# Optimization experiments

Measured on AMD Instinct MI355X. Metric: run time of the kernel, lower is better.

Reference implementation:

```python
import jax, jax.numpy as jnp
import numpy as np

PASS = 8        # pass_through_size
FLOW = 16       # flow_size
TRANS = FLOW - PASS  # transform_size = 8
NBINS = 64
HID = 1024


def _conditioner(yA, w1, b1, w2, b2, w3, b3):
    # MLP producing unnormalized positive bin widths Q: [B, TRANS, NBINS]
    h = jax.nn.relu(yA @ w1 + b1)
    h = jax.nn.relu(h @ w2 + b2)
    q = jax.nn.softplus(h @ w3 + b3) + 1e-6  # positivity for slopes
    return q.reshape(-1, TRANS, NBINS)


def setup_inputs() -> dict:
    key = jax.random.key(0)
    ks = jax.random.split(key, 4)
    B = 65536
    y = jax.random.uniform(ks[0], (B, FLOW + 1), dtype=jnp.float32)
    w1 = jax.random.normal(ks[1], (PASS, HID), dtype=jnp.float32) / np.sqrt(PASS)
    w2 = jax.random.normal(ks[2], (HID, HID), dtype=jnp.float32) / np.sqrt(HID)
    w3 = jax.random.normal(ks[3], (HID, TRANS * NBINS), dtype=jnp.float32) / np.sqrt(HID)
    return {
        "y": y,
        "w1": w1, "b1": jnp.zeros((HID,), jnp.float32),
        "w2": w2, "b2": jnp.zeros((HID,), jnp.float32),
        "w3": w3, "b3": jnp.zeros((TRANS * NBINS,), jnp.float32),
    }


def reference(y, w1, b1, w2, b2, w3, b3):
    yA = y[:, :PASS]                      # [B, PASS]
    yB = y[:, PASS:FLOW]                  # [B, TRANS]
    jac = y[:, FLOW:FLOW + 1]             # [B, 1]

    Q = _conditioner(yA, w1, b1, w2, b2, w3, b3)  # [B, TRANS, NBINS]
    Qsum = jnp.cumsum(Q, axis=-1)
    Qnorms = Qsum[:, :, -1:]
    Q = Q / (Qnorms / NBINS)              # slopes per bin
    Qsum = Qsum / Qnorms                  # normalized CDF knots (last == 1)

    # searchsorted(side='left') per row: count of knots strictly below value
    ybins = jnp.sum(Qsum < yB[..., None], axis=-1)          # [B, TRANS] int32
    ybins = jnp.clip(ybins, 0, NBINS - 1)                   # guard fp edge case

    paddedQsum = jnp.pad(Qsum, ((0, 0), (0, 0), (1, 0)))    # prepend 0 knot
    offsets = jnp.take_along_axis(paddedQsum, ybins[..., None], axis=-1)[..., 0]
    slopes = jnp.take_along_axis(Q, ybins[..., None], axis=-1)[..., 0]

    xB = (yB - offsets) / slopes + ybins.astype(jnp.float32) / NBINS
    jac = jac * jnp.prod(1.0 / slopes, axis=-1, keepdims=True)
    return jnp.concatenate((yA, xB, jac), axis=-1)          # [B, FLOW+1]
```

## Files before the change

kernel.cpp:

```cpp
#include <hip/hip_runtime.h>
#include <hip/hip_bf16.h>
#include <hip/hip_fp16.h>

#define HID 1024
#define QCOLS 512

typedef _Float16 f16x8 __attribute__((ext_vector_type(8)));
typedef float f32x4 __attribute__((ext_vector_type(4)));

__global__ void tconv_split(const float* __restrict__ src, __half* __restrict__ hi,
                            __half* __restrict__ lo, int K, int N, float scale) {
  __shared__ float tile[32][33];
  int n0 = blockIdx.x * 32, k0 = blockIdx.y * 32;
  int tx = threadIdx.x, ty = threadIdx.y;
  for (int i = ty; i < 32; i += 8)
    tile[i][tx] = src[(size_t)(k0 + i) * N + n0 + tx];
  __syncthreads();
  for (int i = ty; i < 32; i += 8) {
    float v = tile[tx][i] * scale;
    __half h = __float2half(v);
    size_t o = (size_t)(n0 + i) * K + k0 + tx;
    hi[o] = h;
    lo[o] = __float2half(v - __half2float(h));
  }
}

__global__ __launch_bounds__(256)
void h1_split(const float* __restrict__ y, const float* __restrict__ w1,
              const float* __restrict__ b1, __half* __restrict__ hi,
              __half* __restrict__ lo, int row0, int nrows) {
  int idx = blockIdx.x * 256 + threadIdx.x;
  if (idx >= nrows * HID) return;
  int r = idx >> 10, c = idx & (HID - 1);
  const float* yr = y + (size_t)(row0 + r) * 17;
  float acc = b1[c];
#pragma unroll
  for (int k = 0; k < 8; ++k) acc = fmaf(yr[k], w1[k * HID + c], acc);
  float v = fmaxf(acc, 0.f) * 64.f;
  __half h = __float2half(v);
  size_t o = (size_t)r * HID + c;
  hi[o] = h;
  lo[o] = __float2half(v - __half2float(h));
}

template <int ACT>
__global__ __launch_bounds__(256)
void gemm_split(const __half* __restrict__ Ahi, const __half* __restrict__ Alo,
                const __half* __restrict__ Bhi, const __half* __restrict__ Blo,
                const float* __restrict__ bias, __half* __restrict__ Chi,
                __half* __restrict__ Clo, float* __restrict__ Cf,
                int M, int N, int K) {
  __shared__ __half lds[4][128 * 32];
  const int tid = threadIdx.x;
  const int wave = tid >> 6, lane = tid & 63;
  const int wr = (wave >> 1) * 64, wc = (wave & 1) * 64;
  const size_t row_blk = (size_t)blockIdx.y * 128;
  const size_t col_blk = (size_t)blockIdx.x * 128;

  f32x4 acc[4][4] = {};

  const int rr_l = lane >> 2;
  const int kk_l = (lane & 3) * 8;

  for (int kt = 0; kt < K; kt += 32) {
    __syncthreads();
#pragma unroll
    for (int j = 0; j < 2; ++j) {
      const int c = wave * 2 + j;
      const int rr = c * 16 + rr_l;
      const size_t ga = (row_blk + rr) * (size_t)K + kt + kk_l;
      const size_t gb = (col_blk + rr) * (size_t)K + kt + kk_l;
      const int lo_off = c * 1024 + lane * 16;
      __builtin_amdgcn_global_load_lds((__attribute__((address_space(1))) void*)(Ahi + ga),
                                       (__attribute__((address_space(3))) void*)((char*)&lds[0][0] + lo_off), 16, 0, 0);
      __builtin_amdgcn_global_load_lds((__attribute__((address_space(1))) void*)(Alo + ga),
                                       (__attribute__((address_space(3))) void*)((char*)&lds[1][0] + lo_off), 16, 0, 0);
      __builtin_amdgcn_global_load_lds((__attribute__((address_space(1))) void*)(Bhi + gb),
                                       (__attribute__((address_space(3))) void*)((char*)&lds[2][0] + lo_off), 16, 0, 0);
      __builtin_amdgcn_global_load_lds((__attribute__((address_space(1))) void*)(Blo + gb),
                                       (__attribute__((address_space(3))) void*)((char*)&lds[3][0] + lo_off), 16, 0, 0);
    }
    __syncthreads();

    const int kb = (lane >> 4) * 16;
    f16x8 ah[4], al[4], bh[4], bl[4];
#pragma unroll
    for (int m = 0; m < 4; ++m) {
      const int rb = (wr + m * 16 + (lane & 15)) * 64 + kb;
      ah[m] = *(const f16x8*)((const char*)&lds[0][0] + rb);
      al[m] = *(const f16x8*)((const char*)&lds[1][0] + rb);
    }
#pragma unroll
    for (int n = 0; n < 4; ++n) {
      const int rb = (wc + n * 16 + (lane & 15)) * 64 + kb;
      bh[n] = *(const f16x8*)((const char*)&lds[2][0] + rb);
      bl[n] = *(const f16x8*)((const char*)&lds[3][0] + rb);
    }
#pragma unroll
    for (int m = 0; m < 4; ++m)
#pragma unroll
      for (int n = 0; n < 4; ++n) {
        acc[m][n] = __builtin_amdgcn_mfma_f32_16x16x32_f16(ah[m], bh[n], acc[m][n], 0, 0, 0);
        acc[m][n] = __builtin_amdgcn_mfma_f32_16x16x32_f16(ah[m], bl[n], acc[m][n], 0, 0, 0);
        acc[m][n] = __builtin_amdgcn_mfma_f32_16x16x32_f16(al[m], bh[n], acc[m][n], 0, 0, 0);
      }
  }

  const float unscale = 1.f / 16384.f;
#pragma unroll
  for (int m = 0; m < 4; ++m) {
    const size_t row_b = row_blk + wr + m * 16 + (lane >> 4) * 4;
#pragma unroll
    for (int n = 0; n < 4; ++n) {
      const size_t col = col_blk + wc + n * 16 + (lane & 15);
      const float bv = bias[col];
#pragma unroll
      for (int j = 0; j < 4; ++j) {
        float v = acc[m][n][j] * unscale + bv;
        const size_t o = (row_b + j) * (size_t)N + col;
        if constexpr (ACT == 0) {
          float r = fmaxf(v, 0.f) * 64.f;
          __half h = __float2half(r);
          Chi[o] = h;
          Clo[o] = __float2half(r - __half2float(h));
        } else {
          float sp = fmaxf(v, 0.f) + log1pf(expf(-fabsf(v)));
          Cf[o] = sp + 1e-6f;
        }
      }
    }
  }
}

__global__ __launch_bounds__(256)
void epilogue_kernel(const float* __restrict__ y, const float* __restrict__ q,
                     float* __restrict__ out, int row0, int nrows) {
  const int wave = threadIdx.x >> 6, lane = threadIdx.x & 63;
  const int r = blockIdx.x * 4 + wave;
  if (r >= nrows) return;
  const float* yr = y + (size_t)(row0 + r) * 17;
  float* orow = out + (size_t)(row0 + r) * 17;
  const float* qr = q + (size_t)r * QCOLS;
  float prod_inv = 1.f;
#pragma unroll
  for (int t = 0; t < 8; ++t) {
    const float qv = qr[t * 64 + lane];
    float s = qv;
#pragma unroll
    for (int d = 1; d < 64; d <<= 1) {
      float u = __shfl_up(s, d);
      if (lane >= d) s += u;
    }
    const float total = __shfl(s, 63);
    const float sn = s / total;
    const float dnorm = total * 0.015625f;
    const float slope_l = qv / dnorm;
    const float yb = yr[8 + t];
    const unsigned long long m = __ballot(sn < yb);
    int bin = (int)__popcll(m);
    bin = bin > 63 ? 63 : bin;
    const float off_g = __shfl(sn, bin > 0 ? bin - 1 : 0);
    const float off = (bin == 0) ? 0.f : off_g;
    const float sl = __shfl(slope_l, bin);
    const float xB = (yb - off) / sl + (float)bin * 0.015625f;
    if (lane == t) orow[8 + t] = xB;
    prod_inv *= (1.f / sl);
  }
  if (lane < 8) orow[lane] = yr[lane];
  if (lane == 8) orow[16] = yr[16] * prod_inv;
}

extern "C" void kernel_launch(void* const* d_in, const int* in_sizes, int n_in,
                              void* d_out, int out_size, void* d_ws, size_t ws_size,
                              hipStream_t stream) {
  const float* y  = (const float*)d_in[0];
  const float* w1 = (const float*)d_in[1];
  const float* b1 = (const float*)d_in[2];
  const float* w2 = (const float*)d_in[3];
  const float* b2 = (const float*)d_in[4];
  const float* w3 = (const float*)d_in[5];
  const float* b3 = (const float*)d_in[6];
  float* out = (float*)d_out;
  const long Btot = in_sizes[0] / 17;

  char* ws = (char*)d_ws;
  __half* w2thi = (__half*)ws;
  __half* w2tlo = (__half*)(ws + (2u << 20));
  __half* w3thi = (__half*)(ws + (4u << 20));
  __half* w3tlo = (__half*)(ws + (5u << 20));
  const size_t fixed = (size_t)6 << 20;

  size_t avail = ws_size > fixed ? ws_size - fixed : 0;
  long maxrows = (long)(avail / 8192);
  long chunk = Btot < maxrows ? Btot : maxrows;
  chunk &= ~127L;
  if (chunk < 128) chunk = 128;

  __half* h1hi = (__half*)(ws + fixed);
  __half* h1lo = (__half*)(ws + fixed + (size_t)chunk * 2048);
  __half* h2hi = (__half*)(ws + fixed + (size_t)chunk * 4096);
  __half* h2lo = (__half*)(ws + fixed + (size_t)chunk * 6144);
  float* qbuf = (float*)h1hi;

  dim3 tb(32, 8);
  tconv_split<<<dim3(HID / 32, HID / 32), tb, 0, stream>>>(w2, w2thi, w2tlo, HID, HID, 256.f);
  tconv_split<<<dim3(QCOLS / 32, HID / 32), tb, 0, stream>>>(w3, w3thi, w3tlo, HID, QCOLS, 256.f);

  for (long row0 = 0; row0 < Btot; row0 += chunk) {
    const int nr = (int)((Btot - row0 < chunk) ? (Btot - row0) : chunk);
    h1_split<<<nr * (HID / 256), 256, 0, stream>>>(y, w1, b1, h1hi, h1lo, (int)row0, nr);
    gemm_split<0><<<dim3(HID / 128, nr / 128), 256, 0, stream>>>(
        h1hi, h1lo, w2thi, w2tlo, b2, h2hi, h2lo, nullptr, nr, HID, HID);
    gemm_split<1><<<dim3(QCOLS / 128, nr / 128), 256, 0, stream>>>(
        h2hi, h2lo, w3thi, w3tlo, b3, nullptr, nullptr, qbuf, nr, QCOLS, HID);
    epilogue_kernel<<<(nr + 3) / 4, 256, 0, stream>>>(y, qbuf, out, (int)row0, nr);
  }
}
```

Baseline: 1.061 ms.

## Rewrite split-fp16 GEMMs as 256x256 double-buffered kernel with interleaved hi/lo layout

Stores the hi and lo fp16 halves of activations and weights interleaved along K (row stride 2048), so the three-product split GEMM becomes a single K=3072 loop over concatenated segments (hi*hi, hi*lo, lo*hi). The new kernel uses 256x256 tiles with 512 threads, double-buffered LDS with XOR swizzling, async global-to-LDS loads overlapped with MFMA, s_setprio, and XCD-aware block remapping. The goal is more data reuse per tile, hiding load latency and avoiding LDS bank conflicts. In exchange it needs 128KB of LDS and heavy register use, and chunks must be multiples of 256 rows.

```diff
diff --git a/kernel.cpp b/kernel.cpp
--- a/kernel.cpp
+++ b/kernel.cpp
@@ -1,15 +1,16 @@
 #include <hip/hip_runtime.h>
-#include <hip/hip_bf16.h>
 #include <hip/hip_fp16.h>
 
 #define HID 1024
 #define QCOLS 512
+#define KP 2048
+#define NT 48
 
 typedef _Float16 f16x8 __attribute__((ext_vector_type(8)));
 typedef float f32x4 __attribute__((ext_vector_type(4)));
 
-__global__ void tconv_split(const float* __restrict__ src, __half* __restrict__ hi,
-                            __half* __restrict__ lo, int K, int N, float scale) {
+__global__ void tconv_split(const float* __restrict__ src, __half* __restrict__ dst,
+                            int K, int N, float scale) {
   __shared__ float tile[32][33];
   int n0 = blockIdx.x * 32, k0 = blockIdx.y * 32;
   int tx = threadIdx.x, ty = threadIdx.y;
@@ -19,16 +20,16 @@
   for (int i = ty; i < 32; i += 8) {
     float v = tile[tx][i] * scale;
     __half h = __float2half(v);
-    size_t o = (size_t)(n0 + i) * K + k0 + tx;
-    hi[o] = h;
-    lo[o] = __float2half(v - __half2float(h));
+    size_t o = (size_t)(n0 + i) * (2 * K) + k0 + tx;
+    dst[o] = h;
+    dst[o + K] = __float2half(v - __half2float(h));
   }
 }
 
 __global__ __launch_bounds__(256)
 void h1_split(const float* __restrict__ y, const float* __restrict__ w1,
-              const float* __restrict__ b1, __half* __restrict__ hi,
-              __half* __restrict__ lo, int row0, int nrows) {
+              const float* __restrict__ b1, __half* __restrict__ h1,
+              int row0, int nrows) {
   int idx = blockIdx.x * 256 + threadIdx.x;
   if (idx >= nrows * HID) return;
   int r = idx >> 10, c = idx & (HID - 1);
@@ -38,91 +39,120 @@
   for (int k = 0; k < 8; ++k) acc = fmaf(yr[k], w1[k * HID + c], acc);
   float v = fmaxf(acc, 0.f) * 64.f;
   __half h = __float2half(v);
-  size_t o = (size_t)r * HID + c;
-  hi[o] = h;
-  lo[o] = __float2half(v - __half2float(h));
+  size_t o = (size_t)r * KP + c;
+  h1[o] = h;
+  h1[o + 1024] = __float2half(v - __half2float(h));
 }
 
 template <int ACT>
-__global__ __launch_bounds__(256)
-void gemm_split(const __half* __restrict__ Ahi, const __half* __restrict__ Alo,
-                const __half* __restrict__ Bhi, const __half* __restrict__ Blo,
-                const float* __restrict__ bias, __half* __restrict__ Chi,
-                __half* __restrict__ Clo, float* __restrict__ Cf,
-                int M, int N, int K) {
-  __shared__ __half lds[4][128 * 32];
+__global__ __launch_bounds__(512, 2)
+void gemm8p(const __half* __restrict__ A, const __half* __restrict__ B,
+            const float* __restrict__ bias, __half* __restrict__ Co,
+            float* __restrict__ Cf, int ldc) {
+  __shared__ char lds[131072];
   const int tid = threadIdx.x;
-  const int wave = tid >> 6, lane = tid & 63;
-  const int wr = (wave >> 1) * 64, wc = (wave & 1) * 64;
-  const size_t row_blk = (size_t)blockIdx.y * 128;
-  const size_t col_blk = (size_t)blockIdx.x * 128;
-
-  f32x4 acc[4][4] = {};
-
-  const int rr_l = lane >> 2;
-  const int kk_l = (lane & 3) * 8;
-
-  for (int kt = 0; kt < K; kt += 32) {
-    __syncthreads();
-#pragma unroll
-    for (int j = 0; j < 2; ++j) {
-      const int c = wave * 2 + j;
-      const int rr = c * 16 + rr_l;
-      const size_t ga = (row_blk + rr) * (size_t)K + kt + kk_l;
-      const size_t gb = (col_blk + rr) * (size_t)K + kt + kk_l;
-      const int lo_off = c * 1024 + lane * 16;
-      __builtin_amdgcn_global_load_lds((__attribute__((address_space(1))) void*)(Ahi + ga),
-                                       (__attribute__((address_space(3))) void*)((char*)&lds[0][0] + lo_off), 16, 0, 0);
-      __builtin_amdgcn_global_load_lds((__attribute__((address_space(1))) void*)(Alo + ga),
-                                       (__attribute__((address_space(3))) void*)((char*)&lds[1][0] + lo_off), 16, 0, 0);
-      __builtin_amdgcn_global_load_lds((__attribute__((address_space(1))) void*)(Bhi + gb),
-                                       (__attribute__((address_space(3))) void*)((char*)&lds[2][0] + lo_off), 16, 0, 0);
-      __builtin_amdgcn_global_load_lds((__attribute__((address_space(1))) void*)(Blo + gb),
-                                       (__attribute__((address_space(3))) void*)((char*)&lds[3][0] + lo_off), 16, 0, 0);
+  const int lane = tid & 63, wave = tid >> 6;
+  const int p = lane & 15, ql = lane >> 4;
+  const int wm = wave >> 2, wn = wave & 3;
+
+  const int gx = gridDim.x, nwg = gx * gridDim.y;
+  const int bid = blockIdx.y * gx + blockIdx.x;
+  const int q8 = nwg >> 3, r8 = nwg & 7;
+  const int xcd = bid & 7, lxi = bid >> 3;
+  const int swz = (xcd < r8 ? xcd * (q8 + 1) : r8 * (q8 + 1) + (xcd - r8) * q8) + lxi;
+  const size_t row_blk = (size_t)(swz / gx) * 256;
+  const size_t col_blk = (size_t)(swz % gx) * 256;
+
+  int a_off[8], b_off[4];
+#pragma unroll
+  for (int m = 0; m < 8; ++m) {
+    int r = wm * 128 + m * 16 + p;
+    a_off[m] = r * 64 + ((ql ^ ((r >> 1) & 3)) << 4);
+  }
+#pragma unroll
+  for (int n = 0; n < 4; ++n) {
+    int r = wn * 64 + n * 16 + p;
+    b_off[n] = r * 64 + ((ql ^ ((r >> 1) & 3)) << 4);
+  }
+
+  const int idx0 = tid, idx1 = tid + 512;
+  const int sr0 = idx0 >> 2, sq0 = (idx0 & 3) ^ ((sr0 >> 1) & 3);
+  const int sr1 = idx1 >> 2, sq1 = (idx1 & 3) ^ ((sr1 >> 1) & 3);
+
+  auto stage = [&](int buf, int h, int kt) {
+    const int lk = kt * 64;
+    const int ak = ((lk >= 2048) ? 1024 : 0) + (lk & 1023) + h * 32;
+    const int bk = ((lk >= 1024 && lk < 2048) ? 1024 : 0) + (lk & 1023) + h * 32;
+    char* pa = lds + buf * 65536 + h * 16384;
+    char* pb = pa + 32768;
+    const __half* ga0 = A + (row_blk + sr0) * (size_t)KP + ak + sq0 * 8;
+    const __half* ga1 = A + (row_blk + sr1) * (size_t)KP + ak + sq1 * 8;
+    const __half* gb0 = B + (col_blk + sr0) * (size_t)KP + bk + sq0 * 8;
+    const __half* gb1 = B + (col_blk + sr1) * (size_t)KP + bk + sq1 * 8;
+    __builtin_amdgcn_global_load_lds((__attribute__((address_space(1))) void*)ga0,
+        (__attribute__((address_space(3))) void*)(pa + idx0 * 16), 16, 0, 0);
+    __builtin_amdgcn_global_load_lds((__attribute__((address_space(1))) void*)ga1,
+        (__attribute__((address_space(3))) void*)(pa + idx1 * 16), 16, 0, 0);
+    __builtin_amdgcn_global_load_lds((__attribute__((address_space(1))) void*)gb0,
+        (__attribute__((address_space(3))) void*)(pb + idx0 * 16), 16, 0, 0);
+    __builtin_amdgcn_global_load_lds((__attribute__((address_space(1))) void*)gb1,
+        (__attribute__((address_space(3))) void*)(pb + idx1 * 16), 16, 0, 0);
+  };
+
+  stage(0, 0, 0);
+  stage(0, 1, 0);
+  asm volatile("s_waitcnt vmcnt(0)" ::: "memory");
+  __builtin_amdgcn_s_barrier();
+
+  f32x4 acc[8][4] = {};
+
+  for (int t = 0; t < NT; ++t) {
+    const int bufp = t & 1;
+    const int ts = (t + 1 < NT) ? t + 1 : NT - 1;
+#pragma unroll
+    for (int h = 0; h < 2; ++h) {
+      const char* pA = lds + bufp * 65536 + h * 16384;
+      const char* pB = pA + 32768;
+      f16x8 af[8], bfr[4];
+#pragma unroll
+      for (int m = 0; m < 8; ++m) af[m] = *(const f16x8*)(pA + a_off[m]);
+#pragma unroll
+      for (int n = 0; n < 4; ++n) bfr[n] = *(const f16x8*)(pB + b_off[n]);
+      stage(bufp ^ 1, h, ts);
+      __builtin_amdgcn_sched_barrier(0);
+      __builtin_amdgcn_s_barrier();
+      __builtin_amdgcn_sched_barrier(0);
+      __builtin_amdgcn_s_setprio(1);
+#pragma unroll
+      for (int m = 0; m < 8; ++m)
+#pragma unroll
+        for (int n = 0; n < 4; ++n)
+          acc[m][n] = __builtin_amdgcn_mfma_f32_16x16x32_f16(af[m], bfr[n], acc[m][n], 0, 0, 0);
+      __builtin_amdgcn_s_setprio(0);
+      asm volatile("s_waitcnt vmcnt(4)" ::: "memory");
+      __builtin_amdgcn_sched_barrier(0);
+      __builtin_amdgcn_s_barrier();
+      __builtin_amdgcn_sched_barrier(0);
     }
-    __syncthreads();
-
-    const int kb = (lane >> 4) * 16;
-    f16x8 ah[4], al[4], bh[4], bl[4];
-#pragma unroll
-    for (int m = 0; m < 4; ++m) {
-      const int rb = (wr + m * 16 + (lane & 15)) * 64 + kb;
-      ah[m] = *(const f16x8*)((const char*)&lds[0][0] + rb);
-      al[m] = *(const f16x8*)((const char*)&lds[1][0] + rb);
-    }
-#pragma unroll
-    for (int n = 0; n < 4; ++n) {
-      const int rb = (wc + n * 16 + (lane & 15)) * 64 + kb;
-      bh[n] = *(const f16x8*)((const char*)&lds[2][0] + rb);
-      bl[n] = *(const f16x8*)((const char*)&lds[3][0] + rb);
-    }
-#pragma unroll
-    for (int m = 0; m < 4; ++m)
-#pragma unroll
-      for (int n = 0; n < 4; ++n) {
-        acc[m][n] = __builtin_amdgcn_mfma_f32_16x16x32_f16(ah[m], bh[n], acc[m][n], 0, 0, 0);
-        acc[m][n] = __builtin_amdgcn_mfma_f32_16x16x32_f16(ah[m], bl[n], acc[m][n], 0, 0, 0);
-        acc[m][n] = __builtin_amdgcn_mfma_f32_16x16x32_f16(al[m], bh[n], acc[m][n], 0, 0, 0);
-      }
   }
 
   const float unscale = 1.f / 16384.f;
 #pragma unroll
-  for (int m = 0; m < 4; ++m) {
-    const size_t row_b = row_blk + wr + m * 16 + (lane >> 4) * 4;
-#pragma unroll
-    for (int n = 0; n < 4; ++n) {
-      const size_t col = col_blk + wc + n * 16 + (lane & 15);
-      const float bv = bias[col];
+  for (int n = 0; n < 4; ++n) {
+    const size_t col = col_blk + wn * 64 + n * 16 + p;
+    const float bv = bias[col];
+#pragma unroll
+    for (int m = 0; m < 8; ++m) {
+      const size_t row0 = row_blk + wm * 128 + m * 16 + ql * 4;
 #pragma unroll
       for (int j = 0; j < 4; ++j) {
         float v = acc[m][n][j] * unscale + bv;
-        const size_t o = (row_b + j) * (size_t)N + col;
+        const size_t o = (row0 + j) * (size_t)ldc + col;
         if constexpr (ACT == 0) {
           float r = fmaxf(v, 0.f) * 64.f;
-          __half h = __float2half(r);
-          Chi[o] = h;
-          Clo[o] = __float2half(r - __half2float(h));
+          __half hh = __float2half(r);
+          Co[o] = hh;
+          Co[o + 1024] = __float2half(r - __half2float(hh));
         } else {
           float sp = fmaxf(v, 0.f) + log1pf(expf(-fabsf(v)));
           Cf[o] = sp + 1e-6f;
@@ -184,35 +214,29 @@
   const long Btot = in_sizes[0] / 17;
 
   char* ws = (char*)d_ws;
-  __half* w2thi = (__half*)ws;
-  __half* w2tlo = (__half*)(ws + (2u << 20));
-  __half* w3thi = (__half*)(ws + (4u << 20));
-  __half* w3tlo = (__half*)(ws + (5u << 20));
+  __half* w2t = (__half*)ws;
+  __half* w3t = (__half*)(ws + (4u << 20));
   const size_t fixed = (size_t)6 << 20;
 
   size_t avail = ws_size > fixed ? ws_size - fixed : 0;
   long maxrows = (long)(avail / 8192);
   long chunk = Btot < maxrows ? Btot : maxrows;
-  chunk &= ~127L;
-  if (chunk < 128) chunk = 128;
-
-  __half* h1hi = (__half*)(ws + fixed);
-  __half* h1lo = (__half*)(ws + fixed + (size_t)chunk * 2048);
-  __half* h2hi = (__half*)(ws + fixed + (size_t)chunk * 4096);
-  __half* h2lo = (__half*)(ws + fixed + (size_t)chunk * 6144);
-  float* qbuf = (float*)h1hi;
+  chunk &= ~255L;
+  if (chunk < 256) chunk = 256;
+
+  __half* h1buf = (__half*)(ws + fixed);
+  __half* h2buf = (__half*)(ws + fixed + (size_t)chunk * 4096);
+  float* qbuf = (float*)h1buf;
 
   dim3 tb(32, 8);
-  tconv_split<<<dim3(HID / 32, HID / 32), tb, 0, stream>>>(w2, w2thi, w2tlo, HID, HID, 256.f);
-  tconv_split<<<dim3(QCOLS / 32, HID / 32), tb, 0, stream>>>(w3, w3thi, w3tlo, HID, QCOLS, 256.f);
+  tconv_split<<<dim3(HID / 32, HID / 32), tb, 0, stream>>>(w2, w2t, HID, HID, 256.f);
+  tconv_split<<<dim3(QCOLS / 32, HID / 32), tb, 0, stream>>>(w3, w3t, HID, QCOLS, 256.f);
 
   for (long row0 = 0; row0 < Btot; row0 += chunk) {
     const int nr = (int)((Btot - row0 < chunk) ? (Btot - row0) : chunk);
-    h1_split<<<nr * (HID / 256), 256, 0, stream>>>(y, w1, b1, h1hi, h1lo, (int)row0, nr);
-    gemm_split<0><<<dim3(HID / 128, nr / 128), 256, 0, stream>>>(
-        h1hi, h1lo, w2thi, w2tlo, b2, h2hi, h2lo, nullptr, nr, HID, HID);
-    gemm_split<1><<<dim3(QCOLS / 128, nr / 128), 256, 0, stream>>>(
-        h2hi, h2lo, w3thi, w3tlo, b3, nullptr, nullptr, qbuf, nr, QCOLS, HID);
+    h1_split<<<nr * (HID / 256), 256, 0, stream>>>(y, w1, b1, h1buf, (int)row0, nr);
+    gemm8p<0><<<dim3(HID / 256, nr / 256), 512, 0, stream>>>(h1buf, w2t, b2, h2buf, nullptr, KP);
+    gemm8p<1><<<dim3(QCOLS / 256, nr / 256), 512, 0, stream>>>(h2buf, w3t, b3, nullptr, qbuf, QCOLS);
     epilogue_kernel<<<(nr + 3) / 4, 256, 0, stream>>>(y, qbuf, out, (int)row0, nr);
   }
 }
```

After: 1.131 ms. +6.6%, slower.
